# Performance work log

Measured on AMD Instinct MI355X. Metric: run time of the kernel, lower is better.

Reference implementation:

```python
import jax, jax.numpy as jnp
import numpy as np

EMBED_DIM = 2048
NUM_HEADS = 16
HEAD_DIM = EMBED_DIM // NUM_HEADS  # 128
GROUP = 256
NEG = -1e9


def setup_inputs() -> dict:
    key = jax.random.key(0)
    ks = jax.random.split(key, 4)
    B, N, C = 2, 8192, EMBED_DIM
    s = 1.0 / np.sqrt(C).astype(np.float32)
    return {
        "x": jax.random.normal(ks[0], (B, N, C), jnp.float32),
        "Wq": jax.random.normal(ks[1], (C, C), jnp.float32) * s,
        "bq": jnp.zeros((C,), jnp.float32),
        "Wk": jax.random.normal(ks[2], (C, C), jnp.float32) * s,
        "bk": jnp.zeros((C,), jnp.float32),
        "Wv": jax.random.normal(ks[3], (C, C), jnp.float32) * s,
        "bv": jnp.zeros((C,), jnp.float32),
    }


def _s2_attn(x, Wq, bq, Wk, bk, Wv, bv):
    B, N, C = x.shape
    H, hd, gs = NUM_HEADS, HEAD_DIM, GROUP
    G = N // gs
    half = H // 2

    def heads(t):  # [B,N,C] -> [B,H,N,hd]
        return t.reshape(B, N, H, hd).transpose(0, 2, 1, 3)

    q = heads(x @ Wq.T + bq)
    k = heads(x @ Wk.T + bk)
    v = heads(x @ Wv.T + bv)

    def shift(t, s):  # shift second half of heads along sequence
        return jnp.concatenate([t[:, :half], jnp.roll(t[:, half:], s, axis=2)], axis=1)

    q, k, v = shift(q, -(gs // 2)), shift(k, -(gs // 2)), shift(v, -(gs // 2))

    # group-local attention: [B,H,G,gs,hd]
    qg = q.reshape(B, H, G, gs, hd)
    kg = k.reshape(B, H, G, gs, hd)
    vg = v.reshape(B, H, G, gs, hd)

    scores = jnp.einsum("bhgqd,bhgkd->bhgqk", qg, kg) / np.sqrt(hd).astype(x.dtype)
    causal = jnp.triu(jnp.ones((gs, gs), bool), 1)  # mask strictly-upper triangle
    scores = jnp.where(causal, NEG, scores)
    attn = jax.nn.softmax(scores, axis=-1)
    out = jnp.einsum("bhgqk,bhgkd->bhgqd", attn, vg).reshape(B, H, N, hd)

    out = shift(out, gs // 2)  # un-shift the shifted heads
    return out.transpose(0, 2, 1, 3).reshape(B, N, C)


def reference(x, Wq, bq, Wk, bk, Wv, bv):
    return _s2_attn(x, Wq, bq, Wk, bk, Wv, bv)
```

## Files before the change

kernel.cpp:

```cpp
#include <hip/hip_runtime.h>
#include <hip/hip_bf16.h>

#define NSEQ 8192
#define CDIM 2048
#define NHEAD 16
#define HD 128

typedef short short8 __attribute__((ext_vector_type(8)));
typedef short short4v __attribute__((ext_vector_type(4)));
typedef float float4v __attribute__((ext_vector_type(4)));

__device__ __forceinline__ short f2bf(float f) {
    __hip_bfloat16 h = __float2bfloat16(f);
    return *reinterpret_cast<short*>(&h);
}

__device__ __forceinline__ void async_load16(const short* g, short* l) {
    __builtin_amdgcn_global_load_lds((const __attribute__((address_space(1))) void*)g,
                                     (__attribute__((address_space(3))) void*)l,
                                     16, 0, 0);
}

#define X8 (33554432 / 8)
#define W8 (4194304 / 8)

__global__ __launch_bounds__(256) void cvt_all(
    const float* __restrict__ x, const float* __restrict__ wq,
    const float* __restrict__ wk, const float* __restrict__ wv,
    short* __restrict__ xb, short* __restrict__ wqb,
    short* __restrict__ wkb, short* __restrict__ wvb)
{
    const size_t i = (size_t)blockIdx.x * blockDim.x + threadIdx.x;
    const float* src;
    short* dst;
    size_t off;
    if (i < X8)              { src = x;  dst = xb;  off = i; }
    else if (i < X8 + W8)    { src = wq; dst = wqb; off = i - X8; }
    else if (i < X8 + 2*W8)  { src = wk; dst = wkb; off = i - X8 - W8; }
    else                     { src = wv; dst = wvb; off = i - X8 - 2*(size_t)W8; }
    const float4v a = ((const float4v*)src)[off * 2];
    const float4v b = ((const float4v*)src)[off * 2 + 1];
    short8 o;
    for (int j = 0; j < 4; j++) { o[j] = f2bf(a[j]); o[4 + j] = f2bf(b[j]); }
    ((short8*)dst)[off] = o;
}

#define PBAR()  asm volatile("s_barrier" ::: "memory")
#define LGKM0() do { asm volatile("s_waitcnt lgkmcnt(0)" ::: "memory"); \
                     __builtin_amdgcn_sched_barrier(0); } while (0)
#define VMC4()  asm volatile("s_waitcnt vmcnt(4)" ::: "memory")

#define MFMA(d, x, y) d = __builtin_amdgcn_mfma_f32_16x16x32_bf16(x, y, d, 0, 0, 0)

__global__ __launch_bounds__(512, 2) void qkv_gemm8(
    const short* __restrict__ xb,
    const short* __restrict__ Wq, const float* __restrict__ bq,
    const short* __restrict__ Wk, const float* __restrict__ bk,
    const short* __restrict__ Wv, const float* __restrict__ bv,
    float* __restrict__ qout, short* __restrict__ kt, short* __restrict__ vt)
{
    __shared__ short lds[2][2][256 * 64];

    const int tid  = threadIdx.x;
    const int w    = tid >> 6;
    const int lane = tid & 63;
    const int quad = lane >> 4;
    const int l15  = lane & 15;
    const int wm   = w >> 2;
    const int wn   = w & 3;

    const int id    = (blockIdx.x & 7) * 192 + (blockIdx.x >> 3);
    const int mtile = id / 24;
    const int rest  = id - mtile * 24;
    const int mat   = rest >> 3;
    const int ntile = rest & 7;
    const int M0 = mtile << 8;
    const int N0 = ntile << 8;

    const short* W    = (mat == 0) ? Wq : (mat == 1) ? Wk : Wv;
    const float* bias = (mat == 0) ? bq : (mat == 1) ? bk : bv;
    const short* Ab = xb + (size_t)M0 * CDIM;
    const short* Bb = W  + (size_t)N0 * CDIM;

    const int stg_row = tid >> 3;
    const int stg_col = ((tid & 7) * 8) ^ (((tid >> 3) & 7) << 3);
    const int cswz    = (lane & 7) << 3;

    float bvals[4];
#pragma unroll
    for (int j = 0; j < 4; ++j)
        bvals[j] = bias[N0 + wn * 64 + j * 16 + l15];
    asm volatile("s_waitcnt vmcnt(0)" ::: "memory");

    float4v acc[8][4];
#pragma unroll
    for (int i = 0; i < 8; ++i)
#pragma unroll
        for (int j = 0; j < 4; ++j)
            acc[i][j] = (float4v){0.f, 0.f, 0.f, 0.f};

    auto stage = [&](int bufi, int ab, int h, int t, const short* src) {
        short* l0 = &lds[bufi][ab][h * 8192 + w * 512];
        const short* g = src + (size_t)(h * 128 + stg_row) * CDIM + t * 64 + stg_col;
        async_load16(g, l0);
        async_load16(g + (size_t)64 * CDIM, l0 + 4096);
    };
    auto ldA = [&](int bufi, int i, int ks) -> short8 {
        const int row = wm * 128 + i * 16 + l15;
        return *(const short8*)&lds[bufi][0][row * 64 + ((ks * 32 + quad * 8) ^ cswz)];
    };
    auto ldB = [&](int bufi, int j, int ks) -> short8 {
        const int row = wn * 64 + j * 16 + l15;
        return *(const short8*)&lds[bufi][1][row * 64 + ((ks * 32 + quad * 8) ^ cswz)];
    };

    stage(0, 0, 0, 0, Ab); stage(0, 0, 1, 0, Ab);
    stage(0, 1, 0, 0, Bb); stage(0, 1, 1, 0, Bb);
    stage(1, 1, 0, 1, Bb); stage(1, 1, 1, 1, Bb);
    VMC4();
    PBAR();

    short8 a[4][2], b[4][2];
    for (int it = 0; it < 16; ++it) {
        const int t1 = 2 * it + 1;
        const int t2 = (2 * it + 2 > 31) ? 31 : 2 * it + 2;
        const int t3 = (2 * it + 3 > 31) ? 31 : 2 * it + 3;

#pragma unroll
        for (int i = 0; i < 4; ++i) { a[i][0] = ldA(0, i, 0); a[i][1] = ldA(0, i, 1); }
#pragma unroll
        for (int j = 0; j < 2; ++j) { b[j][0] = ldB(0, j, 0); b[j][1] = ldB(0, j, 1); }
        stage(1, 0, 0, t1, Ab); stage(1, 0, 1, t1, Ab);
        PBAR(); LGKM0();
        __builtin_amdgcn_s_setprio(1);
#pragma unroll
        for (int i = 0; i < 4; ++i)
#pragma unroll
            for (int j = 0; j < 2; ++j) { MFMA(acc[i][j], a[i][0], b[j][0]);
                                          MFMA(acc[i][j], a[i][1], b[j][1]); }
        __builtin_amdgcn_s_setprio(0);
        PBAR();

#pragma unroll
        for (int j = 2; j < 4; ++j) { b[j][0] = ldB(0, j, 0); b[j][1] = ldB(0, j, 1); }
        PBAR(); LGKM0();
        __builtin_amdgcn_s_setprio(1);
#pragma unroll
        for (int i = 0; i < 4; ++i)
#pragma unroll
            for (int j = 2; j < 4; ++j) { MFMA(acc[i][j], a[i][0], b[j][0]);
                                          MFMA(acc[i][j], a[i][1], b[j][1]); }
        __builtin_amdgcn_s_setprio(0);
        PBAR();

#pragma unroll
        for (int i = 0; i < 4; ++i) { a[i][0] = ldA(0, 4 + i, 0); a[i][1] = ldA(0, 4 + i, 1); }
        stage(0, 1, 0, t2, Bb);
        PBAR(); LGKM0();
        __builtin_amdgcn_s_setprio(1);
#pragma unroll
        for (int i = 0; i < 4; ++i)
#pragma unroll
            for (int j = 2; j < 4; ++j) { MFMA(acc[4 + i][j], a[i][0], b[j][0]);
                                          MFMA(acc[4 + i][j], a[i][1], b[j][1]); }
        __builtin_amdgcn_s_setprio(0);
        PBAR();

        stage(0, 1, 1, t2, Bb);
        PBAR(); LGKM0();
        __builtin_amdgcn_s_setprio(1);
#pragma unroll
        for (int i = 0; i < 4; ++i)
#pragma unroll
            for (int j = 0; j < 2; ++j) { MFMA(acc[4 + i][j], a[i][0], b[j][0]);
                                          MFMA(acc[4 + i][j], a[i][1], b[j][1]); }
        __builtin_amdgcn_s_setprio(0);
        VMC4();
        PBAR();

#pragma unroll
        for (int i = 0; i < 4; ++i) { a[i][0] = ldA(1, i, 0); a[i][1] = ldA(1, i, 1); }
#pragma unroll
        for (int j = 0; j < 2; ++j) { b[j][0] = ldB(1, j, 0); b[j][1] = ldB(1, j, 1); }
        stage(0, 0, 0, t2, Ab); stage(0, 0, 1, t2, Ab);
        PBAR(); LGKM0();
        __builtin_amdgcn_s_setprio(1);
#pragma unroll
        for (int i = 0; i < 4; ++i)
#pragma unroll
            for (int j = 0; j < 2; ++j) { MFMA(acc[i][j], a[i][0], b[j][0]);
                                          MFMA(acc[i][j], a[i][1], b[j][1]); }
        __builtin_amdgcn_s_setprio(0);
        PBAR();

#pragma unroll
        for (int j = 2; j < 4; ++j) { b[j][0] = ldB(1, j, 0); b[j][1] = ldB(1, j, 1); }
        PBAR(); LGKM0();
        __builtin_amdgcn_s_setprio(1);
#pragma unroll
        for (int i = 0; i < 4; ++i)
#pragma unroll
            for (int j = 2; j < 4; ++j) { MFMA(acc[i][j], a[i][0], b[j][0]);
                                          MFMA(acc[i][j], a[i][1], b[j][1]); }
        __builtin_amdgcn_s_setprio(0);
        PBAR();

#pragma unroll
        for (int i = 0; i < 4; ++i) { a[i][0] = ldA(1, 4 + i, 0); a[i][1] = ldA(1, 4 + i, 1); }
        stage(1, 1, 0, t3, Bb);
        PBAR(); LGKM0();
        __builtin_amdgcn_s_setprio(1);
#pragma unroll
        for (int i = 0; i < 4; ++i)
#pragma unroll
            for (int j = 2; j < 4; ++j) { MFMA(acc[4 + i][j], a[i][0], b[j][0]);
                                          MFMA(acc[4 + i][j], a[i][1], b[j][1]); }
        __builtin_amdgcn_s_setprio(0);
        PBAR();

        stage(1, 1, 1, t3, Bb);
        PBAR(); LGKM0();
        __builtin_amdgcn_s_setprio(1);
#pragma unroll
        for (int i = 0; i < 4; ++i)
#pragma unroll
            for (int j = 0; j < 2; ++j) { MFMA(acc[4 + i][j], a[i][0], b[j][0]);
                                          MFMA(acc[4 + i][j], a[i][1], b[j][1]); }
        __builtin_amdgcn_s_setprio(0);
        VMC4();
        PBAR();
    }

#pragma unroll
    for (int j = 0; j < 4; ++j) {
        const int n = N0 + wn * 64 + j * 16 + l15;
        if (mat == 0) {
#pragma unroll
            for (int i = 0; i < 8; ++i) {
                const int mrow = M0 + wm * 128 + i * 16 + quad * 4;
#pragma unroll
                for (int r = 0; r < 4; ++r)
                    qout[((size_t)(mrow + r) << 11) + n] = acc[i][j][r] + bvals[j];
            }
        } else if (mat == 1) {
            const int h = n >> 7;
            const int d = n & (HD - 1);
#pragma unroll
            for (int i = 0; i < 8; ++i) {
                const int mrow = M0 + wm * 128 + i * 16 + quad * 4;
#pragma unroll
                for (int r = 0; r < 4; ++r) {
                    const int m  = mrow + r;
                    const int bb = m >> 13;
                    const int sq = m & (NSEQ - 1);
                    kt[(((size_t)(bb * NHEAD + h) * NSEQ + sq) << 7) + d] =
                        f2bf(acc[i][j][r] + bvals[j]);
                }
            }
        } else {
            const int h = n >> 7;
            const int d = n & (HD - 1);
#pragma unroll
            for (int i = 0; i < 8; ++i) {
                const int mrow = M0 + wm * 128 + i * 16 + quad * 4;
                const int bb = mrow >> 13;
                const int sq = mrow & (NSEQ - 1);
                short4v o4;
#pragma unroll
                for (int r = 0; r < 4; ++r) o4[r] = f2bf(acc[i][j][r] + bvals[j]);
                *(short4v*)&vt[(((size_t)(bb * NHEAD + h) * HD + d) << 13) + sq] = o4;
            }
        }
    }
}

__global__ __launch_bounds__(512, 2) void s2_attn(const float* qsrc,
                                                  const short* __restrict__ kt,
                                                  const short* __restrict__ vt,
                                                  float* out)
{
    __shared__ short Ks[64 * 136];
    __shared__ short Vt[128 * 64];
    __shared__ short Ps[8][32 * 40];

    const int bx = blockIdx.x;
    const int g  = bx & 31;
    const int h  = (bx >> 5) & 15;
    const int b  = bx >> 9;
    const int shift = (h >= 8) ? 128 : 0;
    const int sbase = g * 256 + shift;

    const int tid  = threadIdx.x;
    const int wave = tid >> 6;
    const int lane = tid & 63;
    const int quad = lane >> 4;
    const int l15  = lane & 15;

    const size_t bh = ((size_t)b * NHEAD + h) * NSEQ;
    const short* kg = kt + bh * HD;
    const short* vg = vt + bh * HD;

    const int mt0 = wave * 2;

    short8 qf[2][4];
    for (int im = 0; im < 2; im++) {
        const int row = (mt0 + im) * 16 + l15;
        const int p   = (sbase + row) & (NSEQ - 1);
        const float* qr = qsrc + (((size_t)(b * NSEQ + p)) << 11) + h * HD;
        for (int ks = 0; ks < 4; ks++) {
            const float4v qa = *(const float4v*)(qr + ks * 32 + quad * 8);
            const float4v qb = *(const float4v*)(qr + ks * 32 + quad * 8 + 4);
            short8 f;
            for (int j = 0; j < 4; j++) { f[j] = f2bf(qa[j]); f[4 + j] = f2bf(qb[j]); }
            qf[im][ks] = f;
        }
    }

    const float4v fzero = {0.f, 0.f, 0.f, 0.f};
    float4v o[2][8];
    for (int im = 0; im < 2; im++)
        for (int dt = 0; dt < 8; dt++)
            o[im][dt] = fzero;
    float rs[2][4] = {{0.f, 0.f, 0.f, 0.f}, {0.f, 0.f, 0.f, 0.f}};

    const int vrow_in_w = lane >> 3;
    const int vgcol     = ((lane & 7) * 8) ^ (vrow_in_w << 3);

    for (int kc = 0; kc < 4; kc++) {
        __syncthreads();
        for (int c = 0; c < 2; c++) {
            const int id   = tid + c * 512;
            const int row  = id >> 4;
            const int colb = (id & 15) * 8;
            const int p    = (sbase + kc * 64 + row) & (NSEQ - 1);
            *(short8*)&Ks[row * 136 + colb] = *(const short8*)(kg + (size_t)p * HD + colb);
        }
        for (int c = 0; c < 2; c++) {
            const int d = c * 64 + wave * 8 + vrow_in_w;
            const int p = (sbase + kc * 64 + vgcol) & (NSEQ - 1);
            async_load16(vg + (size_t)d * NSEQ + p, &Vt[(c * 64 + wave * 8) * 64]);
        }
        __syncthreads();

        float4v s[2][4];
        for (int im = 0; im < 2; im++)
            for (int nn = 0; nn < 4; nn++)
                s[im][nn] = fzero;
        for (int nn = 0; nn < 4; nn++) {
            short8 kf[4];
            for (int ks = 0; ks < 4; ks++)
                kf[ks] = *(const short8*)&Ks[(nn * 16 + l15) * 136 + ks * 32 + quad * 8];
            for (int im = 0; im < 2; im++)
                for (int ks = 0; ks < 4; ks++)
                    s[im][nn] = __builtin_amdgcn_mfma_f32_16x16x32_bf16(
                        qf[im][ks], kf[ks], s[im][nn], 0, 0, 0);
        }

        for (int half = 0; half < 2; half++) {
            for (int im = 0; im < 2; im++) {
                const int qpos = (mt0 + im) * 16 + quad * 4;
                for (int nn2 = 0; nn2 < 2; nn2++) {
                    const int nn   = half * 2 + nn2;
                    const int kpos = kc * 64 + nn * 16 + l15;
                    for (int r = 0; r < 4; r++) {
                        const float sv = s[im][nn][r] * 0.088388347648318447f;
                        const float pv = (kpos > qpos + r)
                                             ? 0.f
                                             : __expf(fminf(sv, 30.f));
                        rs[im][r] += pv;
                        Ps[wave][(im * 16 + quad * 4 + r) * 40 + nn2 * 16 + l15] = f2bf(pv);
                    }
                }
            }
            __syncthreads();
            short8 pf[2];
            for (int im = 0; im < 2; im++)
                pf[im] = *(const short8*)&Ps[wave][(im * 16 + l15) * 40 + quad * 8];
            for (int dt = 0; dt < 8; dt++) {
                const int d = dt * 16 + l15;
                const short8 vf = *(const short8*)
                    &Vt[d * 64 + ((half * 32 + quad * 8) ^ ((l15 & 7) << 3))];
                for (int im = 0; im < 2; im++)
                    o[im][dt] = __builtin_amdgcn_mfma_f32_16x16x32_bf16(
                        pf[im], vf, o[im][dt], 0, 0, 0);
            }
            __syncthreads();
        }
    }

    for (int im = 0; im < 2; im++)
        for (int r = 0; r < 4; r++) {
            float v = rs[im][r];
            v += __shfl_xor(v, 1);
            v += __shfl_xor(v, 2);
            v += __shfl_xor(v, 4);
            v += __shfl_xor(v, 8);
            rs[im][r] = v;
        }

    for (int im = 0; im < 2; im++) {
        for (int r = 0; r < 4; r++) {
            const int row = (mt0 + im) * 16 + quad * 4 + r;
            const int p   = (sbase + row) & (NSEQ - 1);
            const float inv = 1.f / rs[im][r];
            const size_t obase = (((size_t)(b * NSEQ + p)) << 11) + h * HD;
            for (int dt = 0; dt < 8; dt++)
                out[obase + dt * 16 + l15] = o[im][dt][r] * inv;
        }
    }
}

extern "C" void kernel_launch(void* const* d_in, const int* in_sizes, int n_in,
                              void* d_out, int out_size, void* d_ws, size_t ws_size,
                              hipStream_t stream) {
    (void)in_sizes; (void)n_in; (void)out_size; (void)ws_size;
    const float* x  = (const float*)d_in[0];
    const float* Wq = (const float*)d_in[1];
    const float* bq = (const float*)d_in[2];
    const float* Wk = (const float*)d_in[3];
    const float* bk = (const float*)d_in[4];
    const float* Wv = (const float*)d_in[5];
    const float* bv = (const float*)d_in[6];

    short* xb  = (short*)d_ws;
    short* wqb = xb  + (size_t)33554432;
    short* wkb = wqb + (size_t)4194304;
    short* wvb = wkb + (size_t)4194304;
    short* kt  = wvb + (size_t)4194304;
    short* vt  = kt  + (size_t)33554432;

    float* outp = (float*)d_out;

    cvt_all<<<dim3(22528), 256, 0, stream>>>(x, Wq, Wk, Wv, xb, wqb, wkb, wvb);
    qkv_gemm8<<<dim3(1536), 512, 0, stream>>>(xb, wqb, bq, wkb, bk, wvb, bv,
                                              outp, kt, vt);
    s2_attn<<<dim3(1024), 512, 0, stream>>>(outp, kt, vt, outp);
}
```

Measured before the change: 767.2 us.

## Software-pipeline K/V tile loads in attention kernel with double-buffered V

The attention kernel now double-buffers the V tile in LDS and prefetches the next K chunk into registers while the current chunk is being computed. This overlaps global loads with MFMA work. Full __syncthreads are replaced by explicit waitcnt/barrier pairs, and the per-wave P buffer sync drops to a local lgkmcnt wait. It also adds s_setprio around the MFMA regions and loosens launch bounds to one block per CU minimum, which risks higher register use and lower occupancy. This kernel is likely a small share of total time next to the QKV GEMM.

```diff
diff --git a/kernel.cpp b/kernel.cpp
--- a/kernel.cpp
+++ b/kernel.cpp
@@ -49,6 +49,7 @@
 #define LGKM0() do { asm volatile("s_waitcnt lgkmcnt(0)" ::: "memory"); \
                      __builtin_amdgcn_sched_barrier(0); } while (0)
 #define VMC4()  asm volatile("s_waitcnt vmcnt(4)" ::: "memory")
+#define VMC0()  asm volatile("s_waitcnt vmcnt(0)" ::: "memory")
 
 #define MFMA(d, x, y) d = __builtin_amdgcn_mfma_f32_16x16x32_bf16(x, y, d, 0, 0, 0)
 
@@ -90,7 +91,7 @@
 #pragma unroll
     for (int j = 0; j < 4; ++j)
         bvals[j] = bias[N0 + wn * 64 + j * 16 + l15];
-    asm volatile("s_waitcnt vmcnt(0)" ::: "memory");
+    VMC0();
 
     float4v acc[8][4];
 #pragma unroll
@@ -274,13 +275,13 @@
     }
 }
 
-__global__ __launch_bounds__(512, 2) void s2_attn(const float* qsrc,
+__global__ __launch_bounds__(512, 1) void s2_attn(const float* qsrc,
                                                   const short* __restrict__ kt,
                                                   const short* __restrict__ vt,
                                                   float* out)
 {
     __shared__ short Ks[64 * 136];
-    __shared__ short Vt[128 * 64];
+    __shared__ short Vt[2][128 * 64];
     __shared__ short Ps[8][32 * 40];
 
     const int bx = blockIdx.x;
@@ -302,15 +303,38 @@
 
     const int mt0 = wave * 2;
 
+    const int vrow_in_w = lane >> 3;
+    const int vgcol     = ((lane & 7) * 8) ^ (vrow_in_w << 3);
+    const int krow0 = tid >> 4;
+    const int kcolb = (tid & 15) * 8;
+
+    short8 kr0, kr1;
+
+    {
+        const int p = (sbase + vgcol) & (NSEQ - 1);
+#pragma unroll
+        for (int c = 0; c < 2; c++) {
+            const int d = c * 64 + wave * 8 + vrow_in_w;
+            async_load16(vg + (size_t)d * NSEQ + p, &Vt[0][(c * 64 + wave * 8) * 64]);
+        }
+        const int p0 = (sbase + krow0) & (NSEQ - 1);
+        const int p1 = (sbase + krow0 + 32) & (NSEQ - 1);
+        kr0 = *(const short8*)(kg + (size_t)p0 * HD + kcolb);
+        kr1 = *(const short8*)(kg + (size_t)p1 * HD + kcolb);
+    }
+
     short8 qf[2][4];
+#pragma unroll
     for (int im = 0; im < 2; im++) {
         const int row = (mt0 + im) * 16 + l15;
         const int p   = (sbase + row) & (NSEQ - 1);
         const float* qr = qsrc + (((size_t)(b * NSEQ + p)) << 11) + h * HD;
+#pragma unroll
         for (int ks = 0; ks < 4; ks++) {
             const float4v qa = *(const float4v*)(qr + ks * 32 + quad * 8);
             const float4v qb = *(const float4v*)(qr + ks * 32 + quad * 8 + 4);
             short8 f;
+#pragma unroll
             for (int j = 0; j < 4; j++) { f[j] = f2bf(qa[j]); f[4 + j] = f2bf(qb[j]); }
             qf[im][ks] = f;
         }
@@ -318,50 +342,66 @@
 
     const float4v fzero = {0.f, 0.f, 0.f, 0.f};
     float4v o[2][8];
+#pragma unroll
     for (int im = 0; im < 2; im++)
+#pragma unroll
         for (int dt = 0; dt < 8; dt++)
             o[im][dt] = fzero;
     float rs[2][4] = {{0.f, 0.f, 0.f, 0.f}, {0.f, 0.f, 0.f, 0.f}};
 
-    const int vrow_in_w = lane >> 3;
-    const int vgcol     = ((lane & 7) * 8) ^ (vrow_in_w << 3);
-
     for (int kc = 0; kc < 4; kc++) {
-        __syncthreads();
-        for (int c = 0; c < 2; c++) {
-            const int id   = tid + c * 512;
-            const int row  = id >> 4;
-            const int colb = (id & 15) * 8;
-            const int p    = (sbase + kc * 64 + row) & (NSEQ - 1);
-            *(short8*)&Ks[row * 136 + colb] = *(const short8*)(kg + (size_t)p * HD + colb);
-        }
-        for (int c = 0; c < 2; c++) {
-            const int d = c * 64 + wave * 8 + vrow_in_w;
-            const int p = (sbase + kc * 64 + vgcol) & (NSEQ - 1);
-            async_load16(vg + (size_t)d * NSEQ + p, &Vt[(c * 64 + wave * 8) * 64]);
-        }
-        __syncthreads();
+        VMC0();
+        *(short8*)&Ks[krow0 * 136 + kcolb]        = kr0;
+        *(short8*)&Ks[(krow0 + 32) * 136 + kcolb] = kr1;
+        LGKM0();
+        PBAR();
+
+        if (kc < 3) {
+            const int p = (sbase + (kc + 1) * 64 + vgcol) & (NSEQ - 1);
+#pragma unroll
+            for (int c = 0; c < 2; c++) {
+                const int d = c * 64 + wave * 8 + vrow_in_w;
+                async_load16(vg + (size_t)d * NSEQ + p,
+                             &Vt[(kc + 1) & 1][(c * 64 + wave * 8) * 64]);
+            }
+            const int p0 = (sbase + (kc + 1) * 64 + krow0) & (NSEQ - 1);
+            const int p1 = (sbase + (kc + 1) * 64 + krow0 + 32) & (NSEQ - 1);
+            kr0 = *(const short8*)(kg + (size_t)p0 * HD + kcolb);
+            kr1 = *(const short8*)(kg + (size_t)p1 * HD + kcolb);
+        }
 
         float4v s[2][4];
+#pragma unroll
         for (int im = 0; im < 2; im++)
+#pragma unroll
             for (int nn = 0; nn < 4; nn++)
                 s[im][nn] = fzero;
+        __builtin_amdgcn_s_setprio(1);
+#pragma unroll
         for (int nn = 0; nn < 4; nn++) {
             short8 kf[4];
+#pragma unroll
             for (int ks = 0; ks < 4; ks++)
                 kf[ks] = *(const short8*)&Ks[(nn * 16 + l15) * 136 + ks * 32 + quad * 8];
+#pragma unroll
             for (int im = 0; im < 2; im++)
+#pragma unroll
                 for (int ks = 0; ks < 4; ks++)
                     s[im][nn] = __builtin_amdgcn_mfma_f32_16x16x32_bf16(
                         qf[im][ks], kf[ks], s[im][nn], 0, 0, 0);
         }
-
+        __builtin_amdgcn_s_setprio(0);
+
+#pragma unroll
         for (int half = 0; half < 2; half++) {
+#pragma unroll
             for (int im = 0; im < 2; im++) {
                 const int qpos = (mt0 + im) * 16 + quad * 4;
+#pragma unroll
                 for (int nn2 = 0; nn2 < 2; nn2++) {
                     const int nn   = half * 2 + nn2;
                     const int kpos = kc * 64 + nn * 16 + l15;
+#pragma unroll
                     for (int r = 0; r < 4; r++) {
                         const float sv = s[im][nn][r] * 0.088388347648318447f;
                         const float pv = (kpos > qpos + r)
@@ -372,23 +412,30 @@
                     }
                 }
             }
-            __syncthreads();
+            LGKM0();
             short8 pf[2];
+#pragma unroll
             for (int im = 0; im < 2; im++)
                 pf[im] = *(const short8*)&Ps[wave][(im * 16 + l15) * 40 + quad * 8];
+            __builtin_amdgcn_s_setprio(1);
+#pragma unroll
             for (int dt = 0; dt < 8; dt++) {
                 const int d = dt * 16 + l15;
                 const short8 vf = *(const short8*)
-                    &Vt[d * 64 + ((half * 32 + quad * 8) ^ ((l15 & 7) << 3))];
+                    &Vt[kc & 1][d * 64 + ((half * 32 + quad * 8) ^ ((l15 & 7) << 3))];
+#pragma unroll
                 for (int im = 0; im < 2; im++)
                     o[im][dt] = __builtin_amdgcn_mfma_f32_16x16x32_bf16(
                         pf[im], vf, o[im][dt], 0, 0, 0);
             }
-            __syncthreads();
-        }
-    }
-
+            __builtin_amdgcn_s_setprio(0);
+        }
+        PBAR();
+    }
+
+#pragma unroll
     for (int im = 0; im < 2; im++)
+#pragma unroll
         for (int r = 0; r < 4; r++) {
             float v = rs[im][r];
             v += __shfl_xor(v, 1);
@@ -398,12 +445,15 @@
             rs[im][r] = v;
         }
 
+#pragma unroll
     for (int im = 0; im < 2; im++) {
+#pragma unroll
         for (int r = 0; r < 4; r++) {
             const int row = (mt0 + im) * 16 + quad * 4 + r;
             const int p   = (sbase + row) & (NSEQ - 1);
             const float inv = 1.f / rs[im][r];
             const size_t obase = (((size_t)(b * NSEQ + p)) << 11) + h * HD;
+#pragma unroll
             for (int dt = 0; dt < 8; dt++)
                 out[obase + dt * 16 + l15] = o[im][dt][r] * inv;
         }
```

Result: faster. 736.6 us (-4.0%).
